# Kernel tuning notes

Measured on AMD Instinct MI355X. Metric: run time of the kernel, lower is better.

Reference implementation:

```python
import jax, jax.numpy as jnp
import numpy as np

N = 8192
F_IN = 512
F_HID = 256
ALPHA = 0.2  # LeakyReLU negative slope
NEG_INF = -9e15


def gat_layer(h, adj, W, a):
    """Standard dense GraphAttentionLayer (pyGAT style).
    h: [N, F_in], adj: [N, N] (0/1), W: [F_in, F_out], a: [2*F_out, 1].
    """
    Wh = h @ W  # [N, F_out]
    f_out = W.shape[1]
    # e_ij = leakyrelu(a1 . Wh_i + a2 . Wh_j) via broadcasting
    e1 = Wh @ a[:f_out]      # [N, 1]
    e2 = Wh @ a[f_out:]      # [N, 1]
    e = jax.nn.leaky_relu(e1 + e2.T, negative_slope=ALPHA)  # [N, N]
    e = jnp.where(adj > 0, e, NEG_INF)
    att = jax.nn.softmax(e, axis=-1)  # masked row softmax
    return jax.nn.elu(att @ Wh)       # [N, F_out]


def setup_inputs() -> dict:
    key = jax.random.key(0)
    k_x, k_adj, k_w1, k_a1, k_w2, k_a2 = jax.random.split(key, 6)
    x = jax.random.normal(k_x, (N, F_IN), dtype=jnp.float32)
    # sparse random adjacency (~avg degree 16) + self loops
    adj = (jax.random.uniform(k_adj, (N, N)) < (16.0 / N)).astype(jnp.float32)
    adj = jnp.clip(adj + jnp.eye(N, dtype=jnp.float32), 0.0, 1.0)
    # Xavier-ish init for layer params
    W1 = jax.random.normal(k_w1, (F_IN, F_HID), dtype=jnp.float32) * (1.0 / np.sqrt(F_IN))
    a1 = jax.random.normal(k_a1, (2 * F_HID, 1), dtype=jnp.float32) * (1.0 / np.sqrt(2 * F_HID))
    W2 = jax.random.normal(k_w2, (F_HID, F_IN), dtype=jnp.float32) * (1.0 / np.sqrt(F_HID))
    a2 = jax.random.normal(k_a2, (2 * F_IN, 1), dtype=jnp.float32) * (1.0 / np.sqrt(2 * F_IN))
    return {"x": x, "adj": adj, "W1": W1, "a1": a1, "W2": W2, "a2": a2}


def reference(x, adj, W1, a1, W2, a2):
    enc = gat_layer(x, adj, W1, a1)    # encode: [N, F_HID]
    dec = gat_layer(enc, adj, W2, a2)  # decode: [N, F_IN]
    return (dec, enc)
```

## Files before the change

### kernel.cpp

```cpp
#include <hip/hip_runtime.h>
#include <hip/hip_bf16.h>

#define N_NODES 8192
#define F_IN    512
#define F_HID   256
#define ALPHA   0.2f
#define MAXDEG  64

using f32x4 = __attribute__((ext_vector_type(4))) float;
using f16x8 = __attribute__((ext_vector_type(8))) _Float16;
using f16x4 = __attribute__((ext_vector_type(4))) _Float16;

__device__ inline void csr_row(const float* __restrict__ adj, int* __restrict__ cols,
                               int* __restrict__ cnt, int row, int lane) {
    const f32x4* arow = (const f32x4*)(adj + (size_t)row * N_NODES);
    int* crow = cols + (size_t)row * MAXDEG;
    int count = 0;
    const unsigned long long mlt = (1ULL << lane) - 1ULL;
    for (int base = 0; base < N_NODES; base += 512) {
        f32x4 v0 = __builtin_nontemporal_load(&arow[(base >> 2) + lane]);
        f32x4 v1 = __builtin_nontemporal_load(&arow[(base >> 2) + 64 + lane]);
        unsigned long long b0 = __ballot(v0[0] > 0.0f);
        unsigned long long b1 = __ballot(v0[1] > 0.0f);
        unsigned long long b2 = __ballot(v0[2] > 0.0f);
        unsigned long long b3 = __ballot(v0[3] > 0.0f);
        unsigned long long b4 = __ballot(v1[0] > 0.0f);
        unsigned long long b5 = __ballot(v1[1] > 0.0f);
        unsigned long long b6 = __ballot(v1[2] > 0.0f);
        unsigned long long b7 = __ballot(v1[3] > 0.0f);
        int o = count + __popcll(b0 & mlt) + __popcll(b1 & mlt)
                      + __popcll(b2 & mlt) + __popcll(b3 & mlt);
        int c0 = base + (lane << 2);
        if (v0[0] > 0.0f) { if (o < MAXDEG) crow[o] = c0;     o++; }
        if (v0[1] > 0.0f) { if (o < MAXDEG) crow[o] = c0 + 1; o++; }
        if (v0[2] > 0.0f) { if (o < MAXDEG) crow[o] = c0 + 2; o++; }
        if (v0[3] > 0.0f) { if (o < MAXDEG) crow[o] = c0 + 3; o++; }
        count += __popcll(b0) + __popcll(b1) + __popcll(b2) + __popcll(b3);
        o = count + __popcll(b4 & mlt) + __popcll(b5 & mlt)
                  + __popcll(b6 & mlt) + __popcll(b7 & mlt);
        int c1 = base + 256 + (lane << 2);
        if (v1[0] > 0.0f) { if (o < MAXDEG) crow[o] = c1;     o++; }
        if (v1[1] > 0.0f) { if (o < MAXDEG) crow[o] = c1 + 1; o++; }
        if (v1[2] > 0.0f) { if (o < MAXDEG) crow[o] = c1 + 2; o++; }
        if (v1[3] > 0.0f) { if (o < MAXDEG) crow[o] = c1 + 3; o++; }
        count += __popcll(b4) + __popcll(b5) + __popcll(b6) + __popcll(b7);
    }
    if (lane == 0) cnt[row] = count > MAXDEG ? MAXDEG : count;
}

__device__ inline void gemm1_tile(const float* __restrict__ x,
                                  const float* __restrict__ W1,
                                  _Float16* __restrict__ Wh1,
                                  const float* __restrict__ a1,
                                  float* __restrict__ s1p, float* __restrict__ t1p,
                                  int brow, int bcol) {
    const int LDT = 72;
    __shared__ _Float16 As[64 * LDT];
    __shared__ _Float16 Bs[128 * LDT];
    const int tid = threadIdx.x;
    const int wid = tid >> 6, lane = tid & 63;
    const int wr = (wid >> 1) * 32, wc = (wid & 1) * 64;
    const int sr = tid >> 3, skg = (tid & 7) * 8;

    f32x4 acc[2][4];
    #pragma unroll
    for (int m = 0; m < 2; ++m)
        #pragma unroll
        for (int n = 0; n < 4; ++n) acc[m][n] = f32x4{0.f, 0.f, 0.f, 0.f};

    for (int k0 = 0; k0 < F_IN; k0 += 64) {
        #pragma unroll
        for (int i = 0; i < 2; ++i) {
            int r = sr + i * 32;
            const f32x4* src = (const f32x4*)(x + (size_t)(brow + r) * F_IN + k0 + skg);
            f32x4 a0 = src[0];
            f32x4 a1v = src[1];
            f16x8 av;
            #pragma unroll
            for (int j = 0; j < 4; ++j) { av[j] = (_Float16)a0[j]; av[4 + j] = (_Float16)a1v[j]; }
            *(f16x8*)&As[r * LDT + skg] = av;
        }
        {
            const int cq = (tid & 31) * 4;
            const int kbase = tid >> 5;
            #pragma unroll
            for (int rd = 0; rd < 8; ++rd) {
                int krow = kbase + 8 * rd;
                f32x4 w = *(const f32x4*)&W1[(size_t)(k0 + krow) * F_HID + bcol + cq];
                #pragma unroll
                for (int q = 0; q < 4; ++q)
                    Bs[(cq + q) * LDT + krow] = (_Float16)w[q];
            }
        }
        __syncthreads();
        #pragma unroll
        for (int ks = 0; ks < 2; ++ks) {
            const int kb = ks * 32 + (lane >> 4) * 8;
            f16x8 af[2], bfr[4];
            #pragma unroll
            for (int m = 0; m < 2; ++m)
                af[m] = *(const f16x8*)&As[(wr + m * 16 + (lane & 15)) * LDT + kb];
            #pragma unroll
            for (int n = 0; n < 4; ++n)
                bfr[n] = *(const f16x8*)&Bs[(wc + n * 16 + (lane & 15)) * LDT + kb];
            #pragma unroll
            for (int m = 0; m < 2; ++m)
                #pragma unroll
                for (int n = 0; n < 4; ++n)
                    acc[m][n] = __builtin_amdgcn_mfma_f32_16x16x32_f16(
                        af[m], bfr[n], acc[m][n], 0, 0, 0);
        }
        __syncthreads();
    }
    const int cl = lane & 15;
    const int part = (bcol >> 7) * 2 + (wc >> 6);
    float as[4], at[4];
    #pragma unroll
    for (int n = 0; n < 4; ++n) {
        as[n] = a1[bcol + wc + n * 16 + cl];
        at[n] = a1[F_HID + bcol + wc + n * 16 + cl];
    }
    #pragma unroll
    for (int m = 0; m < 2; ++m) {
        #pragma unroll
        for (int j = 0; j < 4; ++j) {
            float vs = 0.f, vt = 0.f;
            #pragma unroll
            for (int n = 0; n < 4; ++n) { vs += acc[m][n][j] * as[n]; vt += acc[m][n][j] * at[n]; }
            #pragma unroll
            for (int off = 1; off < 16; off <<= 1) {
                vs += __shfl_xor(vs, off);
                vt += __shfl_xor(vt, off);
            }
            if (cl == 0) {
                int row = brow + wr + m * 16 + ((lane >> 4) << 2) + j;
                s1p[part * N_NODES + row] = vs;
                t1p[part * N_NODES + row] = vt;
            }
        }
        #pragma unroll
        for (int n = 0; n < 4; ++n) {
            int row = brow + wr + m * 16 + ((lane >> 4) << 2);
            int col = bcol + wc + n * 16 + cl;
            #pragma unroll
            for (int j = 0; j < 4; ++j)
                Wh1[(size_t)(row + j) * F_HID + col] = (_Float16)acc[m][n][j];
        }
    }
}

__device__ inline void w2T_tile(int t, const float* __restrict__ W2,
                                _Float16* __restrict__ W2T) {
    __shared__ float Ws[32][33];
    const int kt = t & 7, nt = t >> 3;
    const int tx = threadIdx.x & 31, ty = threadIdx.x >> 5;
    #pragma unroll
    for (int i = 0; i < 4; ++i)
        Ws[ty + 8 * i][tx] = W2[(size_t)(kt * 32 + ty + 8 * i) * F_IN + nt * 32 + tx];
    __syncthreads();
    #pragma unroll
    for (int i = 0; i < 4; ++i)
        W2T[(size_t)(nt * 32 + ty + 8 * i) * F_HID + kt * 32 + tx] = (_Float16)Ws[tx][ty + 8 * i];
}

__device__ inline void w2vec_job(int t, const float* __restrict__ W2,
                                 const float* __restrict__ a2,
                                 float* __restrict__ w2s, float* __restrict__ w2t) {
    const int r = t * 64 + (threadIdx.x >> 2);
    const int q = threadIdx.x & 3;
    float ss = 0.f, tt = 0.f;
    for (int n = q * 4; n < F_IN; n += 16) {
        f32x4 w  = *(const f32x4*)&W2[(size_t)r * F_IN + n];
        f32x4 as = *(const f32x4*)&a2[n];
        f32x4 at = *(const f32x4*)&a2[F_IN + n];
        #pragma unroll
        for (int j = 0; j < 4; ++j) { ss += w[j] * as[j]; tt += w[j] * at[j]; }
    }
    ss += __shfl_xor(ss, 1); ss += __shfl_xor(ss, 2);
    tt += __shfl_xor(tt, 1); tt += __shfl_xor(tt, 2);
    if (q == 0) { w2s[r] = ss; w2t[r] = tt; }
}

__global__ __launch_bounds__(256)
void front_kernel(const float* __restrict__ adj, int* __restrict__ cols,
                  int* __restrict__ cnt, const float* __restrict__ x,
                  const float* __restrict__ W1, const float* __restrict__ a1,
                  _Float16* __restrict__ Wh1,
                  float* __restrict__ s1p, float* __restrict__ t1p,
                  const float* __restrict__ W2, const float* __restrict__ a2,
                  _Float16* __restrict__ W2T,
                  float* __restrict__ w2s, float* __restrict__ w2t) {
    const int bid = blockIdx.x;
    if (bid < 256) {
        gemm1_tile(x, W1, Wh1, a1, s1p, t1p, (bid & 127) * 64, (bid >> 7) * 128);
    } else if (bid < 384) {
        w2T_tile(bid - 256, W2, W2T);
    } else if (bid < 388) {
        w2vec_job(bid - 384, W2, a2, w2s, w2t);
    } else {
        const int q = bid - 388;
        const int row = q * 4 + (threadIdx.x >> 6);
        csr_row(adj, cols, cnt, row, threadIdx.x & 63);
    }
}

__global__ __launch_bounds__(256)
void aggregate_l1(const _Float16* __restrict__ Wh,
                  const int* __restrict__ cols, const int* __restrict__ cnt,
                  const float* __restrict__ s1p, const float* __restrict__ t1p,
                  const float* __restrict__ w2s, const float* __restrict__ w2t,
                  float* __restrict__ enc, _Float16* __restrict__ enc16,
                  float* __restrict__ s2, float* __restrict__ t2) {
    const int wid = threadIdx.x >> 6, lane = threadIdx.x & 63;
    const int row = blockIdx.x * 4 + wid;
    const int deg = cnt[row];
    __shared__ float pS[4][64];
    __shared__ int jS[4][64];
    const float sI = s1p[row] + s1p[N_NODES + row]
                   + s1p[2 * N_NODES + row] + s1p[3 * N_NODES + row];
    int j = 0;
    float ev = -1e30f;
    if (lane < deg) {
        j = cols[(size_t)row * MAXDEG + lane];
        float tj = t1p[j] + t1p[N_NODES + j]
                 + t1p[2 * N_NODES + j] + t1p[3 * N_NODES + j];
        float z = sI + tj;
        ev = z > 0.0f ? z : ALPHA * z;
    }
    float m = ev;
    #pragma unroll
    for (int off = 32; off > 0; off >>= 1) m = fmaxf(m, __shfl_xor(m, off));
    float ex = (lane < deg) ? __expf(ev - m) : 0.0f;
    float sum = ex;
    #pragma unroll
    for (int off = 32; off > 0; off >>= 1) sum += __shfl_xor(sum, off);
    pS[wid][lane] = ex / sum;
    jS[wid][lane] = j;
    __syncthreads();

    float acc[4] = {};
    const size_t lo = (size_t)lane * 4;
    int d = 0;
    for (; d + 4 <= deg; d += 4) {
        float p0 = pS[wid][d],     p1 = pS[wid][d + 1];
        float p2 = pS[wid][d + 2], p3 = pS[wid][d + 3];
        f16x4 v0 = *(const f16x4*)(Wh + (size_t)jS[wid][d] * F_HID + lo);
        f16x4 v1 = *(const f16x4*)(Wh + (size_t)jS[wid][d + 1] * F_HID + lo);
        f16x4 v2 = *(const f16x4*)(Wh + (size_t)jS[wid][d + 2] * F_HID + lo);
        f16x4 v3 = *(const f16x4*)(Wh + (size_t)jS[wid][d + 3] * F_HID + lo);
        #pragma unroll
        for (int jj = 0; jj < 4; ++jj)
            acc[jj] += p0 * (float)v0[jj] + p1 * (float)v1[jj]
                     + p2 * (float)v2[jj] + p3 * (float)v3[jj];
    }
    for (; d < deg; ++d) {
        float p = pS[wid][d];
        f16x4 w = *(const f16x4*)(Wh + (size_t)jS[wid][d] * F_HID + lo);
        #pragma unroll
        for (int jj = 0; jj < 4; ++jj) acc[jj] += p * (float)w[jj];
    }
    f32x4 o; f16x4 h;
    #pragma unroll
    for (int jj = 0; jj < 4; ++jj) {
        float v = acc[jj];
        float e = v > 0.0f ? v : (__expf(v) - 1.0f);
        o[jj] = e; h[jj] = (_Float16)e;
    }
    __builtin_nontemporal_store(o, (f32x4*)(enc + (size_t)row * F_HID + lo));
    *(f16x4*)(enc16 + (size_t)row * F_HID + lo) = h;

    f32x4 ws = *(const f32x4*)(w2s + lo);
    f32x4 wt = *(const f32x4*)(w2t + lo);
    float ps = 0.f, pt = 0.f;
    #pragma unroll
    for (int jj = 0; jj < 4; ++jj) { ps += o[jj] * ws[jj]; pt += o[jj] * wt[jj]; }
    #pragma unroll
    for (int off = 32; off > 0; off >>= 1) {
        ps += __shfl_xor(ps, off);
        pt += __shfl_xor(pt, off);
    }
    if (lane == 0) { s2[row] = ps; t2[row] = pt; }
}

__global__ __launch_bounds__(256)
void aggregate_l2pre(const _Float16* __restrict__ enc16,
                     const int* __restrict__ cols, const int* __restrict__ cnt,
                     const float* __restrict__ s, const float* __restrict__ t,
                     _Float16* __restrict__ aggE16) {
    const int wid = threadIdx.x >> 6, lane = threadIdx.x & 63;
    const int row = blockIdx.x * 4 + wid;
    const int deg = cnt[row];
    __shared__ float pS[4][64];
    __shared__ int jS[4][64];
    int j = 0;
    float ev = -1e30f;
    if (lane < deg) {
        j = cols[(size_t)row * MAXDEG + lane];
        float z = s[row] + t[j];
        ev = z > 0.0f ? z : ALPHA * z;
    }
    float m = ev;
    #pragma unroll
    for (int off = 32; off > 0; off >>= 1) m = fmaxf(m, __shfl_xor(m, off));
    float ex = (lane < deg) ? __expf(ev - m) : 0.0f;
    float sum = ex;
    #pragma unroll
    for (int off = 32; off > 0; off >>= 1) sum += __shfl_xor(sum, off);
    pS[wid][lane] = ex / sum;
    jS[wid][lane] = j;
    __syncthreads();

    float acc[4] = {};
    const size_t lo = (size_t)lane * 4;
    int d = 0;
    for (; d + 4 <= deg; d += 4) {
        float p0 = pS[wid][d],     p1 = pS[wid][d + 1];
        float p2 = pS[wid][d + 2], p3 = pS[wid][d + 3];
        f16x4 v0 = *(const f16x4*)(enc16 + (size_t)jS[wid][d] * F_HID + lo);
        f16x4 v1 = *(const f16x4*)(enc16 + (size_t)jS[wid][d + 1] * F_HID + lo);
        f16x4 v2 = *(const f16x4*)(enc16 + (size_t)jS[wid][d + 2] * F_HID + lo);
        f16x4 v3 = *(const f16x4*)(enc16 + (size_t)jS[wid][d + 3] * F_HID + lo);
        #pragma unroll
        for (int jj = 0; jj < 4; ++jj)
            acc[jj] += p0 * (float)v0[jj] + p1 * (float)v1[jj]
                     + p2 * (float)v2[jj] + p3 * (float)v3[jj];
    }
    for (; d < deg; ++d) {
        float p = pS[wid][d];
        f16x4 w = *(const f16x4*)(enc16 + (size_t)jS[wid][d] * F_HID + lo);
        #pragma unroll
        for (int jj = 0; jj < 4; ++jj) acc[jj] += p * (float)w[jj];
    }
    f16x4 h;
    #pragma unroll
    for (int jj = 0; jj < 4; ++jj) h[jj] = (_Float16)acc[jj];
    *(f16x4*)(aggE16 + (size_t)row * F_HID + lo) = h;
}

__global__ __launch_bounds__(256)
void gemm2e(const _Float16* __restrict__ A, const _Float16* __restrict__ BT,
            float* __restrict__ C) {
    const int LDT = 72, LDB = 264;
    __shared__ _Float16 As[128 * LDT];
    __shared__ _Float16 Bs[64 * LDB];
    const int tid = threadIdx.x;
    const int wid = tid >> 6, lane = tid & 63;
    const int brow = (blockIdx.x >> 3) * 128;
    const int bcol = (blockIdx.x & 7) * 64;
    const int wr = (wid >> 1) * 64, wc = (wid & 1) * 32;

    #pragma unroll
    for (int i = 0; i < 8; ++i) {
        int id = tid + i * 256;
        int r = id >> 5, kc = (id & 31) * 8;
        *(f16x8*)&Bs[r * LDB + kc] = *(const f16x8*)&BT[(size_t)(bcol + r) * F_HID + kc];
    }

    f32x4 acc[4][2];
    #pragma unroll
    for (int m = 0; m < 4; ++m)
        #pragma unroll
        for (int n = 0; n < 2; ++n) acc[m][n] = f32x4{0.f, 0.f, 0.f, 0.f};

    for (int k0 = 0; k0 < F_HID; k0 += 64) {
        #pragma unroll
        for (int i = 0; i < 4; ++i) {
            int id = tid + i * 256;
            int r = id >> 3, kc = (id & 7) * 8;
            *(f16x8*)&As[r * LDT + kc] = *(const f16x8*)&A[(size_t)(brow + r) * F_HID + k0 + kc];
        }
        __syncthreads();
        #pragma unroll
        for (int ks = 0; ks < 2; ++ks) {
            const int kb = ks * 32 + (lane >> 4) * 8;
            f16x8 af[4], bfr[2];
            #pragma unroll
            for (int m = 0; m < 4; ++m)
                af[m] = *(const f16x8*)&As[(wr + m * 16 + (lane & 15)) * LDT + kb];
            #pragma unroll
            for (int n = 0; n < 2; ++n)
                bfr[n] = *(const f16x8*)&Bs[(wc + n * 16 + (lane & 15)) * LDB + k0 + kb];
            #pragma unroll
            for (int m = 0; m < 4; ++m)
                #pragma unroll
                for (int n = 0; n < 2; ++n)
                    acc[m][n] = __builtin_amdgcn_mfma_f32_16x16x32_f16(
                        af[m], bfr[n], acc[m][n], 0, 0, 0);
        }
        __syncthreads();
    }
    #pragma unroll
    for (int m = 0; m < 4; ++m)
        #pragma unroll
        for (int n = 0; n < 2; ++n) {
            int row = brow + wr + m * 16 + ((lane >> 4) << 2);
            int col = bcol + wc + n * 16 + (lane & 15);
            #pragma unroll
            for (int j = 0; j < 4; ++j) {
                float v = acc[m][n][j];
                float e = v > 0.0f ? v : (__expf(v) - 1.0f);
                __builtin_nontemporal_store(e, &C[(size_t)(row + j) * F_IN + col]);
            }
        }
}

extern "C" void kernel_launch(void* const* d_in, const int* in_sizes, int n_in,
                              void* d_out, int out_size, void* d_ws, size_t ws_size,
                              hipStream_t stream) {
    (void)in_sizes; (void)n_in; (void)out_size; (void)ws_size;
    const float* x   = (const float*)d_in[0];
    const float* adj = (const float*)d_in[1];
    const float* W1  = (const float*)d_in[2];
    const float* a1  = (const float*)d_in[3];
    const float* W2  = (const float*)d_in[4];
    const float* a2  = (const float*)d_in[5];

    float* dec = (float*)d_out;
    float* enc = dec + (size_t)N_NODES * F_IN;

    int*      cols   = (int*)d_ws;
    int*      cnt    = cols + (size_t)N_NODES * MAXDEG;
    float*    s1p    = (float*)(cnt + N_NODES);
    float*    t1p    = s1p + 4 * N_NODES;
    float*    s2     = t1p + 4 * N_NODES;
    float*    t2     = s2 + N_NODES;
    float*    w2s    = t2 + N_NODES;
    float*    w2t    = w2s + F_HID;
    _Float16* Wh1    = (_Float16*)(w2t + F_HID);
    _Float16* enc16  = Wh1 + (size_t)N_NODES * F_HID;
    _Float16* aggE16 = enc16 + (size_t)N_NODES * F_HID;
    _Float16* W2T    = aggE16 + (size_t)N_NODES * F_HID;

    front_kernel<<<2436, 256, 0, stream>>>(adj, cols, cnt, x, W1, a1, Wh1,
                                           s1p, t1p, W2, a2, W2T, w2s, w2t);

    aggregate_l1<<<N_NODES / 4, 256, 0, stream>>>(Wh1, cols, cnt, s1p, t1p,
                                                  w2s, w2t, enc, enc16, s2, t2);

    aggregate_l2pre<<<N_NODES / 4, 256, 0, stream>>>(enc16, cols, cnt, s2, t2, aggE16);

    gemm2e<<<512, 256, 0, stream>>>(aggE16, W2T, dec);
}
```

Baseline: 99.10 us.

## Split adjacency CSR scan across kernels to overlap with layer-1 aggregation

The dense adjacency-to-CSR scan is split in half. The front kernel now scans only the first 4096 rows. A new mid kernel scans the remaining rows while other blocks aggregate layer 1 for the first half of the rows, whose CSR is already complete. A third kernel then aggregates the second half. The aim is to hide the layer-1 aggregation behind the bandwidth-bound adjacency read, at the cost of one extra kernel launch and the removal of the block-level barrier around the per-wave shared buffers.

```diff
diff --git a/kernel.cpp b/kernel.cpp
--- a/kernel.cpp
+++ b/kernel.cpp
@@ -181,6 +181,81 @@
     if (q == 0) { w2s[r] = ss; w2t[r] = tt; }
 }
 
+__device__ inline void agg_l1_quad(int q, const _Float16* __restrict__ Wh,
+                                   const int* __restrict__ cols, const int* __restrict__ cnt,
+                                   const float* __restrict__ s1p, const float* __restrict__ t1p,
+                                   const float* __restrict__ w2s, const float* __restrict__ w2t,
+                                   float* __restrict__ enc, _Float16* __restrict__ enc16,
+                                   float* __restrict__ s2, float* __restrict__ t2,
+                                   float (*pS)[64], int (*jS)[64]) {
+    const int wid = threadIdx.x >> 6, lane = threadIdx.x & 63;
+    const int row = q * 4 + wid;
+    const int deg = cnt[row];
+    const float sI = s1p[row] + s1p[N_NODES + row]
+                   + s1p[2 * N_NODES + row] + s1p[3 * N_NODES + row];
+    int j = 0;
+    float ev = -1e30f;
+    if (lane < deg) {
+        j = cols[(size_t)row * MAXDEG + lane];
+        float tj = t1p[j] + t1p[N_NODES + j]
+                 + t1p[2 * N_NODES + j] + t1p[3 * N_NODES + j];
+        float z = sI + tj;
+        ev = z > 0.0f ? z : ALPHA * z;
+    }
+    float m = ev;
+    #pragma unroll
+    for (int off = 32; off > 0; off >>= 1) m = fmaxf(m, __shfl_xor(m, off));
+    float ex = (lane < deg) ? __expf(ev - m) : 0.0f;
+    float sum = ex;
+    #pragma unroll
+    for (int off = 32; off > 0; off >>= 1) sum += __shfl_xor(sum, off);
+    pS[wid][lane] = ex / sum;
+    jS[wid][lane] = j;
+
+    float acc[4] = {};
+    const size_t lo = (size_t)lane * 4;
+    int d = 0;
+    for (; d + 4 <= deg; d += 4) {
+        float p0 = pS[wid][d],     p1 = pS[wid][d + 1];
+        float p2 = pS[wid][d + 2], p3 = pS[wid][d + 3];
+        f16x4 v0 = *(const f16x4*)(Wh + (size_t)jS[wid][d] * F_HID + lo);
+        f16x4 v1 = *(const f16x4*)(Wh + (size_t)jS[wid][d + 1] * F_HID + lo);
+        f16x4 v2 = *(const f16x4*)(Wh + (size_t)jS[wid][d + 2] * F_HID + lo);
+        f16x4 v3 = *(const f16x4*)(Wh + (size_t)jS[wid][d + 3] * F_HID + lo);
+        #pragma unroll
+        for (int jj = 0; jj < 4; ++jj)
+            acc[jj] += p0 * (float)v0[jj] + p1 * (float)v1[jj]
+                     + p2 * (float)v2[jj] + p3 * (float)v3[jj];
+    }
+    for (; d < deg; ++d) {
+        float p = pS[wid][d];
+        f16x4 w = *(const f16x4*)(Wh + (size_t)jS[wid][d] * F_HID + lo);
+        #pragma unroll
+        for (int jj = 0; jj < 4; ++jj) acc[jj] += p * (float)w[jj];
+    }
+    f32x4 o; f16x4 h;
+    #pragma unroll
+    for (int jj = 0; jj < 4; ++jj) {
+        float v = acc[jj];
+        float e = v > 0.0f ? v : (__expf(v) - 1.0f);
+        o[jj] = e; h[jj] = (_Float16)e;
+    }
+    __builtin_nontemporal_store(o, (f32x4*)(enc + (size_t)row * F_HID + lo));
+    *(f16x4*)(enc16 + (size_t)row * F_HID + lo) = h;
+
+    f32x4 ws = *(const f32x4*)(w2s + lo);
+    f32x4 wt = *(const f32x4*)(w2t + lo);
+    float ps = 0.f, pt = 0.f;
+    #pragma unroll
+    for (int jj = 0; jj < 4; ++jj) { ps += o[jj] * ws[jj]; pt += o[jj] * wt[jj]; }
+    #pragma unroll
+    for (int off = 32; off > 0; off >>= 1) {
+        ps += __shfl_xor(ps, off);
+        pt += __shfl_xor(pt, off);
+    }
+    if (lane == 0) { s2[row] = ps; t2[row] = pt; }
+}
+
 __global__ __launch_bounds__(256)
 void front_kernel(const float* __restrict__ adj, int* __restrict__ cols,
                   int* __restrict__ cnt, const float* __restrict__ x,
@@ -205,81 +280,36 @@
 }
 
 __global__ __launch_bounds__(256)
-void aggregate_l1(const _Float16* __restrict__ Wh,
-                  const int* __restrict__ cols, const int* __restrict__ cnt,
-                  const float* __restrict__ s1p, const float* __restrict__ t1p,
-                  const float* __restrict__ w2s, const float* __restrict__ w2t,
-                  float* __restrict__ enc, _Float16* __restrict__ enc16,
-                  float* __restrict__ s2, float* __restrict__ t2) {
-    const int wid = threadIdx.x >> 6, lane = threadIdx.x & 63;
-    const int row = blockIdx.x * 4 + wid;
-    const int deg = cnt[row];
+void mid_kernel(const float* __restrict__ adj, int* __restrict__ cols,
+                int* __restrict__ cnt, const _Float16* __restrict__ Wh1,
+                const float* __restrict__ s1p, const float* __restrict__ t1p,
+                const float* __restrict__ w2s, const float* __restrict__ w2t,
+                float* __restrict__ enc, _Float16* __restrict__ enc16,
+                float* __restrict__ s2, float* __restrict__ t2) {
     __shared__ float pS[4][64];
     __shared__ int jS[4][64];
-    const float sI = s1p[row] + s1p[N_NODES + row]
-                   + s1p[2 * N_NODES + row] + s1p[3 * N_NODES + row];
-    int j = 0;
-    float ev = -1e30f;
-    if (lane < deg) {
-        j = cols[(size_t)row * MAXDEG + lane];
-        float tj = t1p[j] + t1p[N_NODES + j]
-                 + t1p[2 * N_NODES + j] + t1p[3 * N_NODES + j];
-        float z = sI + tj;
-        ev = z > 0.0f ? z : ALPHA * z;
-    }
-    float m = ev;
-    #pragma unroll
-    for (int off = 32; off > 0; off >>= 1) m = fmaxf(m, __shfl_xor(m, off));
-    float ex = (lane < deg) ? __expf(ev - m) : 0.0f;
-    float sum = ex;
-    #pragma unroll
-    for (int off = 32; off > 0; off >>= 1) sum += __shfl_xor(sum, off);
-    pS[wid][lane] = ex / sum;
-    jS[wid][lane] = j;
-    __syncthreads();
-
-    float acc[4] = {};
-    const size_t lo = (size_t)lane * 4;
-    int d = 0;
-    for (; d + 4 <= deg; d += 4) {
-        float p0 = pS[wid][d],     p1 = pS[wid][d + 1];
-        float p2 = pS[wid][d + 2], p3 = pS[wid][d + 3];
-        f16x4 v0 = *(const f16x4*)(Wh + (size_t)jS[wid][d] * F_HID + lo);
-        f16x4 v1 = *(const f16x4*)(Wh + (size_t)jS[wid][d + 1] * F_HID + lo);
-        f16x4 v2 = *(const f16x4*)(Wh + (size_t)jS[wid][d + 2] * F_HID + lo);
-        f16x4 v3 = *(const f16x4*)(Wh + (size_t)jS[wid][d + 3] * F_HID + lo);
-        #pragma unroll
-        for (int jj = 0; jj < 4; ++jj)
-            acc[jj] += p0 * (float)v0[jj] + p1 * (float)v1[jj]
-                     + p2 * (float)v2[jj] + p3 * (float)v3[jj];
-    }
-    for (; d < deg; ++d) {
-        float p = pS[wid][d];
-        f16x4 w = *(const f16x4*)(Wh + (size_t)jS[wid][d] * F_HID + lo);
-        #pragma unroll
-        for (int jj = 0; jj < 4; ++jj) acc[jj] += p * (float)w[jj];
-    }
-    f32x4 o; f16x4 h;
-    #pragma unroll
-    for (int jj = 0; jj < 4; ++jj) {
-        float v = acc[jj];
-        float e = v > 0.0f ? v : (__expf(v) - 1.0f);
-        o[jj] = e; h[jj] = (_Float16)e;
-    }
-    __builtin_nontemporal_store(o, (f32x4*)(enc + (size_t)row * F_HID + lo));
-    *(f16x4*)(enc16 + (size_t)row * F_HID + lo) = h;
-
-    f32x4 ws = *(const f32x4*)(w2s + lo);
-    f32x4 wt = *(const f32x4*)(w2t + lo);
-    float ps = 0.f, pt = 0.f;
-    #pragma unroll
-    for (int jj = 0; jj < 4; ++jj) { ps += o[jj] * ws[jj]; pt += o[jj] * wt[jj]; }
-    #pragma unroll
-    for (int off = 32; off > 0; off >>= 1) {
-        ps += __shfl_xor(ps, off);
-        pt += __shfl_xor(pt, off);
-    }
-    if (lane == 0) { s2[row] = ps; t2[row] = pt; }
+    const int bid = blockIdx.x;
+    if (bid < 1024) {
+        const int q = 1024 + bid;
+        const int row = q * 4 + (threadIdx.x >> 6);
+        csr_row(adj, cols, cnt, row, threadIdx.x & 63);
+    } else {
+        agg_l1_quad(bid - 1024, Wh1, cols, cnt, s1p, t1p, w2s, w2t,
+                    enc, enc16, s2, t2, pS, jS);
+    }
+}
+
+__global__ __launch_bounds__(256)
+void agg1_rest(const _Float16* __restrict__ Wh1,
+               const int* __restrict__ cols, const int* __restrict__ cnt,
+               const float* __restrict__ s1p, const float* __restrict__ t1p,
+               const float* __restrict__ w2s, const float* __restrict__ w2t,
+               float* __restrict__ enc, _Float16* __restrict__ enc16,
+               float* __restrict__ s2, float* __restrict__ t2) {
+    __shared__ float pS[4][64];
+    __shared__ int jS[4][64];
+    agg_l1_quad(1024 + blockIdx.x, Wh1, cols, cnt, s1p, t1p, w2s, w2t,
+                enc, enc16, s2, t2, pS, jS);
 }
 
 __global__ __launch_bounds__(256)
@@ -431,11 +461,14 @@
     _Float16* aggE16 = enc16 + (size_t)N_NODES * F_HID;
     _Float16* W2T    = aggE16 + (size_t)N_NODES * F_HID;
 
-    front_kernel<<<2436, 256, 0, stream>>>(adj, cols, cnt, x, W1, a1, Wh1,
+    front_kernel<<<1412, 256, 0, stream>>>(adj, cols, cnt, x, W1, a1, Wh1,
                                            s1p, t1p, W2, a2, W2T, w2s, w2t);
 
-    aggregate_l1<<<N_NODES / 4, 256, 0, stream>>>(Wh1, cols, cnt, s1p, t1p,
-                                                  w2s, w2t, enc, enc16, s2, t2);
+    mid_kernel<<<2048, 256, 0, stream>>>(adj, cols, cnt, Wh1, s1p, t1p,
+                                         w2s, w2t, enc, enc16, s2, t2);
+
+    agg1_rest<<<1024, 256, 0, stream>>>(Wh1, cols, cnt, s1p, t1p,
+                                        w2s, w2t, enc, enc16, s2, t2);
 
     aggregate_l2pre<<<N_NODES / 4, 256, 0, stream>>>(enc16, cols, cnt, s2, t2, aggE16);
 
```

New measurement: 102.1 us. +3.0%, slower.

## Overlap second-layer aggregation with the first half of the output GEMM

Applied to the files above, without the earlier changes.

Splits the layer-2 aggregation and the output GEMM into three launches. The first aggregates rows 0-4095. The second runs GEMM tiles for those rows alongside aggregation of rows 4096-8191 in one heterogeneous kernel. The third finishes the remaining GEMM tiles. The aim is to overlap the memory-bound gather with MFMA work and reduce idle tail time. The cost is an extra launch, plus shared memory sized for the GEMM in every block, which lowers occupancy for the aggregation blocks. The __syncthreads was dropped, which is safe only because each wave reads just its own pS/jS row.

```diff
diff --git a/kernel.cpp b/kernel.cpp
--- a/kernel.cpp
+++ b/kernel.cpp
@@ -282,16 +282,14 @@
     if (lane == 0) { s2[row] = ps; t2[row] = pt; }
 }
 
-__global__ __launch_bounds__(256)
-void aggregate_l2pre(const _Float16* __restrict__ enc16,
-                     const int* __restrict__ cols, const int* __restrict__ cnt,
-                     const float* __restrict__ s, const float* __restrict__ t,
-                     _Float16* __restrict__ aggE16) {
+__device__ inline void agg_l2_quad(int q, const _Float16* __restrict__ enc16,
+                                   const int* __restrict__ cols, const int* __restrict__ cnt,
+                                   const float* __restrict__ s, const float* __restrict__ t,
+                                   _Float16* __restrict__ aggE16,
+                                   float (*pS)[64], int (*jS)[64]) {
     const int wid = threadIdx.x >> 6, lane = threadIdx.x & 63;
-    const int row = blockIdx.x * 4 + wid;
+    const int row = q * 4 + wid;
     const int deg = cnt[row];
-    __shared__ float pS[4][64];
-    __shared__ int jS[4][64];
     int j = 0;
     float ev = -1e30f;
     if (lane < deg) {
@@ -308,7 +306,6 @@
     for (int off = 32; off > 0; off >>= 1) sum += __shfl_xor(sum, off);
     pS[wid][lane] = ex / sum;
     jS[wid][lane] = j;
-    __syncthreads();
 
     float acc[4] = {};
     const size_t lo = (size_t)lane * 4;
@@ -337,16 +334,15 @@
     *(f16x4*)(aggE16 + (size_t)row * F_HID + lo) = h;
 }
 
-__global__ __launch_bounds__(256)
-void gemm2e(const _Float16* __restrict__ A, const _Float16* __restrict__ BT,
-            float* __restrict__ C) {
+__device__ inline void gemm2e_tile(int tile, const _Float16* __restrict__ A,
+                                   const _Float16* __restrict__ BT,
+                                   float* __restrict__ C,
+                                   _Float16* As, _Float16* Bs) {
     const int LDT = 72, LDB = 264;
-    __shared__ _Float16 As[128 * LDT];
-    __shared__ _Float16 Bs[64 * LDB];
     const int tid = threadIdx.x;
     const int wid = tid >> 6, lane = tid & 63;
-    const int brow = (blockIdx.x >> 3) * 128;
-    const int bcol = (blockIdx.x & 7) * 64;
+    const int brow = (tile >> 3) * 128;
+    const int bcol = (tile & 7) * 64;
     const int wr = (wid >> 1) * 64, wc = (wid & 1) * 32;
 
     #pragma unroll
@@ -402,6 +398,42 @@
                 __builtin_nontemporal_store(e, &C[(size_t)(row + j) * F_IN + col]);
             }
         }
+}
+
+__global__ __launch_bounds__(256)
+void agg2_first(const _Float16* __restrict__ enc16,
+                const int* __restrict__ cols, const int* __restrict__ cnt,
+                const float* __restrict__ s2, const float* __restrict__ t2,
+                _Float16* __restrict__ aggE16) {
+    __shared__ float pS[4][64];
+    __shared__ int jS[4][64];
+    agg_l2_quad(blockIdx.x, enc16, cols, cnt, s2, t2, aggE16, pS, jS);
+}
+
+__global__ __launch_bounds__(256)
+void cd_kernel(const _Float16* __restrict__ enc16, const _Float16* __restrict__ W2T,
+               const int* __restrict__ cols, const int* __restrict__ cnt,
+               const float* __restrict__ s2, const float* __restrict__ t2,
+               _Float16* __restrict__ aggE16, float* __restrict__ dec) {
+    __shared__ __align__(16) char smem[128 * 72 * 2 + 64 * 264 * 2];
+    const int bid = blockIdx.x;
+    if (bid < 256) {
+        _Float16* As = (_Float16*)smem;
+        _Float16* Bs = (_Float16*)(smem + 128 * 72 * 2);
+        gemm2e_tile(bid, aggE16, W2T, dec, As, Bs);
+    } else {
+        float (*pS)[64] = (float(*)[64])smem;
+        int (*jS)[64] = (int(*)[64])(smem + 1024);
+        agg_l2_quad(1024 + (bid - 256), enc16, cols, cnt, s2, t2, aggE16, pS, jS);
+    }
+}
+
+__global__ __launch_bounds__(256)
+void gemm2_rest(const _Float16* __restrict__ aggE16, const _Float16* __restrict__ W2T,
+                float* __restrict__ dec) {
+    __shared__ __align__(16) _Float16 As[128 * 72];
+    __shared__ __align__(16) _Float16 Bs[64 * 264];
+    gemm2e_tile(256 + blockIdx.x, aggE16, W2T, dec, As, Bs);
 }
 
 extern "C" void kernel_launch(void* const* d_in, const int* in_sizes, int n_in,
@@ -437,7 +469,9 @@
     aggregate_l1<<<N_NODES / 4, 256, 0, stream>>>(Wh1, cols, cnt, s1p, t1p,
                                                   w2s, w2t, enc, enc16, s2, t2);
 
-    aggregate_l2pre<<<N_NODES / 4, 256, 0, stream>>>(enc16, cols, cnt, s2, t2, aggE16);
-
-    gemm2e<<<512, 256, 0, stream>>>(aggE16, W2T, dec);
-}
+    agg2_first<<<1024, 256, 0, stream>>>(enc16, cols, cnt, s2, t2, aggE16);
+
+    cd_kernel<<<1280, 256, 0, stream>>>(enc16, W2T, cols, cnt, s2, t2, aggE16, dec);
+
+    gemm2_rest<<<256, 256, 0, stream>>>(aggE16, W2T, dec);
+}
```

After: 104.3 us. 5.3% more time.
